# Kernel tuning notes

Hardware: AMD Instinct MI355X
Metric: run time of the kernel (lower is better)

The kernel has to match this reference:

```python
import jax, jax.numpy as jnp
import numpy as np

N_EMBED = 8192
EMBED_DIM = 4
BETA = 0.25


def setup_inputs() -> dict:
    key = jax.random.key(0)
    k1, k2 = jax.random.split(key)
    z = jax.random.normal(k1, (8, EMBED_DIM, 64, 64), dtype=jnp.float32)
    # torch init: uniform(-1/n_embed, 1/n_embed)
    embed_w = jax.random.uniform(k2, (N_EMBED, EMBED_DIM), dtype=jnp.float32,
                                 minval=-1.0 / N_EMBED, maxval=1.0 / N_EMBED)
    return {"z": z, "embed_w": embed_w}


def reference(z, embed_w):
    # z: [B, C, H, W] -> [B, H, W, C]
    z_nhwc = jnp.transpose(z, (0, 2, 3, 1))
    z_flat = z_nhwc.reshape(-1, EMBED_DIM)  # [N, D]
    # squared L2 distances: ||z||^2 + ||e||^2 - 2 z e^T  -> [N, n_embed]
    d = (jnp.sum(z_flat * z_flat, axis=1, keepdims=True)
         + jnp.sum(embed_w * embed_w, axis=1)
         - 2.0 * z_flat @ embed_w.T)
    min_idx = jnp.argmin(d, axis=1)  # [N] int
    z_q = embed_w[min_idx].reshape(z_nhwc.shape)  # [B, H, W, C]
    sg = jax.lax.stop_gradient
    loss = (jnp.mean((sg(z_q) - z_nhwc) ** 2)
            + BETA * jnp.mean((z_q - sg(z_nhwc)) ** 2))
    # straight-through estimator
    z_q_ste = z_nhwc + sg(z_q - z_nhwc)
    z_q_out = jnp.transpose(z_q_ste, (0, 3, 1, 2))  # back to [B, C, H, W]
    return z_q_out, loss, min_idx
```

## Files before the change

kernel.cpp:

```cpp
#include <hip/hip_runtime.h>
#include <hip/hip_bf16.h>
#include <math.h>

typedef __attribute__((ext_vector_type(8))) short bf16x8;
typedef __attribute__((ext_vector_type(4))) float f32x4;
typedef __attribute__((ext_vector_type(4))) int i32x4;

#define N_POINTS 32768
#define NUM_EMBED 8192
#define CH 64
#define CPC (NUM_EMBED / CH)
#define CSTRIDE 4096

__device__ __forceinline__ unsigned int bfr(float f) {
    __hip_bfloat16 h = __float2bfloat16(f);
    return (unsigned int)*reinterpret_cast<unsigned short*>(&h);
}
__device__ __forceinline__ uint2 pack4(float a, float b, float c, float d) {
    return make_uint2(bfr(a) | (bfr(b) << 16), bfr(c) | (bfr(d) << 16));
}

__device__ __forceinline__ unsigned int fkey(float f) {
    unsigned int b = __float_as_uint(f);
    return b ^ (0x80000000u | (unsigned int)((int)b >> 31));
}

__global__ void vq_pack_kernel(const float4* __restrict__ E, uint2* __restrict__ ebf) {
    int i = blockIdx.x * 256 + threadIdx.x;
    if (i < NUM_EMBED) {
        float4 e = E[i];
        ebf[i] = pack4(e.x, e.y, e.z, e.w);
    }
}

__global__ __launch_bounds__(256) void vq_fused_kernel(
        const float* __restrict__ z, const uint2* __restrict__ ebf,
        const float4* __restrict__ E,
        float* __restrict__ out, double* __restrict__ partial) {
    __shared__ float sCm[CH][17];
    __shared__ double sLoss[16];
    const int lane = threadIdx.x & 63;
    const int wid = threadIdx.x >> 6;
    const int n0 = blockIdx.x * 16;

    const bool lo = lane < 16;
    {
        int n = n0 + (lane & 15);
        int b = n >> 12, hw = n & 4095;
        const float* zp = z + b * 16384 + hw;
        uint2 zl = pack4(zp[0], zp[CSTRIDE], zp[2 * CSTRIDE], zp[3 * CSTRIDE]);
        i32x4 bi = { lo ? (int)zl.x : 0, lo ? (int)zl.y : 0, 0, 0 };
        bf16x8 bfrag = *(bf16x8*)&bi;
        const f32x4 zero4 = {0.f, 0.f, 0.f, 0.f};

        for (int ci = 0; ci < 16; ++ci) {
            int c = wid * 16 + ci;
            float rm = -__builtin_inff();
            #pragma unroll
            for (int t = 0; t < 8; ++t) {
                int j0 = (c * 8 + t) * 16;
                uint2 el = ebf[j0 + (lane & 15)];
                i32x4 ai = { lo ? (int)el.x : 0, lo ? (int)el.y : 0, 0, 0 };
                bf16x8 afrag = *(bf16x8*)&ai;
                f32x4 d = __builtin_amdgcn_mfma_f32_16x16x32_bf16(afrag, bfrag, zero4, 0, 0, 0);
                rm = fmaxf(rm, fmaxf(fmaxf(d[0], d[1]), fmaxf(d[2], d[3])));
            }
            rm = fmaxf(rm, __shfl_xor(rm, 16));
            rm = fmaxf(rm, __shfl_xor(rm, 32));
            if (lo) sCm[c][lane] = rm;
        }
    }
    __syncthreads();

    for (int q = 0; q < 4; ++q) {
        int pl = wid * 4 + q;
        int n = n0 + pl;
        int b = n >> 12, hw = n & 4095;
        const float* zp = z + b * 16384 + hw;
        float z0 = zp[0];
        float z1 = zp[CSTRIDE];
        float z2 = zp[2 * CSTRIDE];
        float z3 = zp[3 * CSTRIDE];
        float zz = __fmul_rn(z0, z0);
        zz = __fadd_rn(zz, __fmul_rn(z1, z1));
        zz = __fadd_rn(zz, __fmul_rn(z2, z2));
        zz = __fadd_rn(zz, __fmul_rn(z3, z3));

        float cm = sCm[lane][pl];
        float gmax = cm;
        #pragma unroll
        for (int off = 32; off; off >>= 1)
            gmax = fmaxf(gmax, __shfl_xor(gmax, off));

        float u = __fmul_rn(__fadd_rn(zz, 0.01f), 2.38418579e-07f);
        float L1 = __fadd_rn(__fadd_rn(fabsf(z0), fabsf(z1)),
                             __fadd_rn(fabsf(z2), fabsf(z3)));
        float slack = __fadd_rn(__fadd_rn(u, u), __fmaf_rn(L1, 2.0e-6f, 2.0e-7f));
        float thr = __fsub_rn(gmax, slack);
        unsigned long long mask = __ballot(cm >= thr);

        unsigned long long bkey = ~0ull;
        while (mask) {
            int c = __builtin_ctzll(mask);
            mask &= mask - 1ull;
            int j0 = c * CPC + lane;
            #pragma unroll
            for (int h = 0; h < 2; ++h) {
                int j = j0 + h * 64;
                float4 e = E[j];
                float ee = __fmul_rn(e.x, e.x);
                ee = __fadd_rn(ee, __fmul_rn(e.y, e.y));
                ee = __fadd_rn(ee, __fmul_rn(e.z, e.z));
                ee = __fadd_rn(ee, __fmul_rn(e.w, e.w));
                float dot = __fmul_rn(z0, e.x);
                dot = __fmaf_rn(z1, e.y, dot);
                dot = __fmaf_rn(z2, e.z, dot);
                dot = __fmaf_rn(z3, e.w, dot);
                float d = __fmaf_rn(-2.0f, dot, __fadd_rn(zz, ee));
                unsigned long long key =
                    ((unsigned long long)fkey(d) << 32) | (unsigned int)j;
                bkey = key < bkey ? key : bkey;
            }
        }
        #pragma unroll
        for (int off = 32; off; off >>= 1) {
            unsigned long long o = __shfl_xor(bkey, off);
            bkey = o < bkey ? o : bkey;
        }
        int besti = (int)(unsigned int)(bkey & 0xFFFFFFFFull);

        if (lane == 0) {
            float4 e = E[besti];
            float* op = out + b * 16384 + hw;
            float t0 = __fsub_rn(e.x, z0);
            float t1 = __fsub_rn(e.y, z1);
            float t2 = __fsub_rn(e.z, z2);
            float t3 = __fsub_rn(e.w, z3);
            op[0]           = __fadd_rn(z0, t0);
            op[CSTRIDE]     = __fadd_rn(z1, t1);
            op[2 * CSTRIDE] = __fadd_rn(z2, t2);
            op[3 * CSTRIDE] = __fadd_rn(z3, t3);
            out[131073 + n] = (float)besti;
            sLoss[pl] = (double)__fmul_rn(t0, t0) + (double)__fmul_rn(t1, t1)
                      + (double)__fmul_rn(t2, t2) + (double)__fmul_rn(t3, t3);
        }
    }
    __syncthreads();
    if (threadIdx.x == 0) {
        double s = 0.0;
        #pragma unroll
        for (int w = 0; w < 16; ++w) s += sLoss[w];
        partial[blockIdx.x] = s;
    }
}

__global__ void vq_loss_kernel(const double* __restrict__ partial, float* __restrict__ out) {
    __shared__ double sdata[256];
    int t = threadIdx.x;
    double s = 0.0;
    for (int i = t; i < 2048; i += 256) s += partial[i];
    sdata[t] = s;
    __syncthreads();
    #pragma unroll
    for (int st = 128; st > 0; st >>= 1) {
        if (t < st) sdata[t] += sdata[t + st];
        __syncthreads();
    }
    if (t == 0) {
        float m = (float)(sdata[0] / 131072.0);
        out[131072] = __fadd_rn(m, __fmul_rn(0.25f, m));
    }
}

extern "C" void kernel_launch(void* const* d_in, const int* in_sizes, int n_in,
                              void* d_out, int out_size, void* d_ws, size_t ws_size,
                              hipStream_t stream) {
    const float* z = (const float*)d_in[0];
    const float4* E = (const float4*)d_in[1];
    float* out = (float*)d_out;

    char* ws = (char*)d_ws;
    uint2* ebf = (uint2*)ws;
    double* partial = (double*)(ws + 65536);

    vq_pack_kernel<<<NUM_EMBED / 256, 256, 0, stream>>>(E, ebf);
    vq_fused_kernel<<<N_POINTS / 16, 256, 0, stream>>>(z, ebf, E, out, partial);
    vq_loss_kernel<<<1, 256, 0, stream>>>(partial, out);
}
```

Before: 59.79 us.

## Replace bf16 MFMA chunk-max prefilter with fp32 VALU dot products

```diff
diff --git a/kernel.cpp b/kernel.cpp
--- a/kernel.cpp
+++ b/kernel.cpp
@@ -1,10 +1,5 @@
 #include <hip/hip_runtime.h>
-#include <hip/hip_bf16.h>
 #include <math.h>
-
-typedef __attribute__((ext_vector_type(8))) short bf16x8;
-typedef __attribute__((ext_vector_type(4))) float f32x4;
-typedef __attribute__((ext_vector_type(4))) int i32x4;
 
 #define N_POINTS 32768
 #define NUM_EMBED 8192
@@ -12,63 +7,49 @@
 #define CPC (NUM_EMBED / CH)
 #define CSTRIDE 4096
 
-__device__ __forceinline__ unsigned int bfr(float f) {
-    __hip_bfloat16 h = __float2bfloat16(f);
-    return (unsigned int)*reinterpret_cast<unsigned short*>(&h);
-}
-__device__ __forceinline__ uint2 pack4(float a, float b, float c, float d) {
-    return make_uint2(bfr(a) | (bfr(b) << 16), bfr(c) | (bfr(d) << 16));
-}
-
 __device__ __forceinline__ unsigned int fkey(float f) {
     unsigned int b = __float_as_uint(f);
     return b ^ (0x80000000u | (unsigned int)((int)b >> 31));
 }
 
-__global__ void vq_pack_kernel(const float4* __restrict__ E, uint2* __restrict__ ebf) {
-    int i = blockIdx.x * 256 + threadIdx.x;
-    if (i < NUM_EMBED) {
-        float4 e = E[i];
-        ebf[i] = pack4(e.x, e.y, e.z, e.w);
-    }
-}
-
 __global__ __launch_bounds__(256) void vq_fused_kernel(
-        const float* __restrict__ z, const uint2* __restrict__ ebf,
-        const float4* __restrict__ E,
+        const float* __restrict__ z, const float4* __restrict__ E,
         float* __restrict__ out, double* __restrict__ partial) {
     __shared__ float sCm[CH][17];
     __shared__ double sLoss[16];
     const int lane = threadIdx.x & 63;
     const int wid = threadIdx.x >> 6;
     const int n0 = blockIdx.x * 16;
+    const int cs = lane & 15;
+    const int pt = wid * 4 + (lane >> 4);
 
-    const bool lo = lane < 16;
+    float z0, z1, z2, z3;
     {
-        int n = n0 + (lane & 15);
+        int n = n0 + pt;
         int b = n >> 12, hw = n & 4095;
         const float* zp = z + b * 16384 + hw;
-        uint2 zl = pack4(zp[0], zp[CSTRIDE], zp[2 * CSTRIDE], zp[3 * CSTRIDE]);
-        i32x4 bi = { lo ? (int)zl.x : 0, lo ? (int)zl.y : 0, 0, 0 };
-        bf16x8 bfrag = *(bf16x8*)&bi;
-        const f32x4 zero4 = {0.f, 0.f, 0.f, 0.f};
+        z0 = zp[0];
+        z1 = zp[CSTRIDE];
+        z2 = zp[2 * CSTRIDE];
+        z3 = zp[3 * CSTRIDE];
+    }
 
-        for (int ci = 0; ci < 16; ++ci) {
-            int c = wid * 16 + ci;
-            float rm = -__builtin_inff();
-            #pragma unroll
-            for (int t = 0; t < 8; ++t) {
-                int j0 = (c * 8 + t) * 16;
-                uint2 el = ebf[j0 + (lane & 15)];
-                i32x4 ai = { lo ? (int)el.x : 0, lo ? (int)el.y : 0, 0, 0 };
-                bf16x8 afrag = *(bf16x8*)&ai;
-                f32x4 d = __builtin_amdgcn_mfma_f32_16x16x32_bf16(afrag, bfrag, zero4, 0, 0, 0);
-                rm = fmaxf(rm, fmaxf(fmaxf(d[0], d[1]), fmaxf(d[2], d[3])));
-            }
-            rm = fmaxf(rm, __shfl_xor(rm, 16));
-            rm = fmaxf(rm, __shfl_xor(rm, 32));
-            if (lo) sCm[c][lane] = rm;
+    for (int c = 0; c < CH; ++c) {
+        float rm = -__builtin_inff();
+        #pragma unroll
+        for (int t = 0; t < 8; ++t) {
+            float4 e = E[c * CPC + t * 16 + cs];
+            float dot = __fmul_rn(z0, e.x);
+            dot = __fmaf_rn(z1, e.y, dot);
+            dot = __fmaf_rn(z2, e.z, dot);
+            dot = __fmaf_rn(z3, e.w, dot);
+            rm = fmaxf(rm, dot);
         }
+        rm = fmaxf(rm, __shfl_xor(rm, 1));
+        rm = fmaxf(rm, __shfl_xor(rm, 2));
+        rm = fmaxf(rm, __shfl_xor(rm, 4));
+        rm = fmaxf(rm, __shfl_xor(rm, 8));
+        if (cs == 0) sCm[c][pt] = rm;
     }
     __syncthreads();
 
@@ -77,14 +58,14 @@
         int n = n0 + pl;
         int b = n >> 12, hw = n & 4095;
         const float* zp = z + b * 16384 + hw;
-        float z0 = zp[0];
-        float z1 = zp[CSTRIDE];
-        float z2 = zp[2 * CSTRIDE];
-        float z3 = zp[3 * CSTRIDE];
-        float zz = __fmul_rn(z0, z0);
-        zz = __fadd_rn(zz, __fmul_rn(z1, z1));
-        zz = __fadd_rn(zz, __fmul_rn(z2, z2));
-        zz = __fadd_rn(zz, __fmul_rn(z3, z3));
+        float y0 = zp[0];
+        float y1 = zp[CSTRIDE];
+        float y2 = zp[2 * CSTRIDE];
+        float y3 = zp[3 * CSTRIDE];
+        float zz = __fmul_rn(y0, y0);
+        zz = __fadd_rn(zz, __fmul_rn(y1, y1));
+        zz = __fadd_rn(zz, __fmul_rn(y2, y2));
+        zz = __fadd_rn(zz, __fmul_rn(y3, y3));
 
         float cm = sCm[lane][pl];
         float gmax = cm;
@@ -93,10 +74,7 @@
             gmax = fmaxf(gmax, __shfl_xor(gmax, off));
 
         float u = __fmul_rn(__fadd_rn(zz, 0.01f), 2.38418579e-07f);
-        float L1 = __fadd_rn(__fadd_rn(fabsf(z0), fabsf(z1)),
-                             __fadd_rn(fabsf(z2), fabsf(z3)));
-        float slack = __fadd_rn(__fadd_rn(u, u), __fmaf_rn(L1, 2.0e-6f, 2.0e-7f));
-        float thr = __fsub_rn(gmax, slack);
+        float thr = __fsub_rn(gmax, __fadd_rn(__fadd_rn(u, u), 1e-7f));
         unsigned long long mask = __ballot(cm >= thr);
 
         unsigned long long bkey = ~0ull;
@@ -112,10 +90,10 @@
                 ee = __fadd_rn(ee, __fmul_rn(e.y, e.y));
                 ee = __fadd_rn(ee, __fmul_rn(e.z, e.z));
                 ee = __fadd_rn(ee, __fmul_rn(e.w, e.w));
-                float dot = __fmul_rn(z0, e.x);
-                dot = __fmaf_rn(z1, e.y, dot);
-                dot = __fmaf_rn(z2, e.z, dot);
-                dot = __fmaf_rn(z3, e.w, dot);
+                float dot = __fmul_rn(y0, e.x);
+                dot = __fmaf_rn(y1, e.y, dot);
+                dot = __fmaf_rn(y2, e.z, dot);
+                dot = __fmaf_rn(y3, e.w, dot);
                 float d = __fmaf_rn(-2.0f, dot, __fadd_rn(zz, ee));
                 unsigned long long key =
                     ((unsigned long long)fkey(d) << 32) | (unsigned int)j;
@@ -132,14 +110,14 @@
         if (lane == 0) {
             float4 e = E[besti];
             float* op = out + b * 16384 + hw;
-            float t0 = __fsub_rn(e.x, z0);
-            float t1 = __fsub_rn(e.y, z1);
-            float t2 = __fsub_rn(e.z, z2);
-            float t3 = __fsub_rn(e.w, z3);
-            op[0]           = __fadd_rn(z0, t0);
-            op[CSTRIDE]     = __fadd_rn(z1, t1);
-            op[2 * CSTRIDE] = __fadd_rn(z2, t2);
-            op[3 * CSTRIDE] = __fadd_rn(z3, t3);
+            float t0 = __fsub_rn(e.x, y0);
+            float t1 = __fsub_rn(e.y, y1);
+            float t2 = __fsub_rn(e.z, y2);
+            float t3 = __fsub_rn(e.w, y3);
+            op[0]           = __fadd_rn(y0, t0);
+            op[CSTRIDE]     = __fadd_rn(y1, t1);
+            op[2 * CSTRIDE] = __fadd_rn(y2, t2);
+            op[3 * CSTRIDE] = __fadd_rn(y3, t3);
             out[131073 + n] = (float)besti;
             sLoss[pl] = (double)__fmul_rn(t0, t0) + (double)__fmul_rn(t1, t1)
                       + (double)__fmul_rn(t2, t2) + (double)__fmul_rn(t3, t3);
@@ -179,11 +157,8 @@
     const float4* E = (const float4*)d_in[1];
     float* out = (float*)d_out;
 
-    char* ws = (char*)d_ws;
-    uint2* ebf = (uint2*)ws;
-    double* partial = (double*)(ws + 65536);
+    double* partial = (double*)d_ws;
 
-    vq_pack_kernel<<<NUM_EMBED / 256, 256, 0, stream>>>(E, ebf);
-    vq_fused_kernel<<<N_POINTS / 16, 256, 0, stream>>>(z, ebf, E, out, partial);
+    vq_fused_kernel<<<N_POINTS / 16, 256, 0, stream>>>(z, E, out, partial);
     vq_loss_kernel<<<1, 256, 0, stream>>>(partial, out);
 }
```

Result: slower. 134.4 us (+124.8%).
